# Kernel optimization log

Hardware: AMD Instinct MI355X
Metric: run time of the kernel (lower is better)

Reference implementation:

```python
import jax, jax.numpy as jnp
import numpy as np
from jax import lax


def _gelu(x):
    return jax.nn.gelu(x, approximate=False)  # torch nn.GELU default = exact erf


def _ln_cf(x, g, b, eps=1e-6):
    # channels_first LayerNorm over dim 1 (biased variance, as in the source)
    m = x.mean(1, keepdims=True)
    v = ((x - m) ** 2).mean(1, keepdims=True)
    return g[None, :, None, None] * ((x - m) / jnp.sqrt(v + eps)) + b[None, :, None, None]


def _conv1x1(x, w):
    return jnp.einsum('bihw,oi->bohw', x, w[:, :, 0, 0])


def _conv3x3(x, w, d):
    # 3x3 conv, padding=dilation=d, no bias
    return lax.conv_general_dilated(x, w, (1, 1), [(d, d), (d, d)], rhs_dilation=(d, d),
                                    dimension_numbers=('NCHW', 'OIHW', 'NCHW'))


def _forward(x, conv1_w, conv1_b, conv2_w, conv2_b,
             cw_w1, cw_b1, cw_ln_g, cw_ln_b, cw_w2, cw_b2,
             aspp0_w, aspp0_g, aspp0_b, aspp1_w, aspp1_g, aspp1_b,
             aspp2_w, aspp2_g, aspp2_b, aspp3_w, aspp3_g, aspp3_b,
             asppp_w, asppp_g, asppp_b, proj_w, proj_g, proj_b):
    B, C, H, W = x.shape
    # x1 = conv1(x)
    x1 = _conv1x1(x, conv1_w) + conv1_b[None, :, None, None]
    # ChannelWeighting
    avg = x.mean((2, 3))                                    # [B,C]
    mx = x.max((2, 3))
    o = jnp.abs(avg - mx) * avg
    h = o @ cw_w1.T + cw_b1                                 # [B,Cout]
    mu = h.mean(-1, keepdims=True)
    vv = ((h - mu) ** 2).mean(-1, keepdims=True)
    h = cw_ln_g * ((h - mu) / jnp.sqrt(vv + 1e-5)) + cw_ln_b  # nn.LayerNorm eps=1e-5
    s = jax.nn.sigmoid(h @ cw_w2.T + cw_b2)                 # [B,C]
    xc = x * s[:, :, None, None] + x
    # ASPP (dropout in project is identity at eval)
    b0 = _gelu(_ln_cf(_conv1x1(xc, aspp0_w), aspp0_g, aspp0_b))
    b1 = _gelu(_ln_cf(_conv3x3(xc, aspp1_w, 3), aspp1_g, aspp1_b))
    b2 = _gelu(_ln_cf(_conv3x3(xc, aspp2_w, 6), aspp2_g, aspp2_b))
    b3 = _gelu(_ln_cf(_conv3x3(xc, aspp3_w, 9), aspp3_g, aspp3_b))
    gp = xc.mean((2, 3), keepdims=True)                     # AdaptiveAvgPool2d(1)
    bp = _gelu(_ln_cf(_conv1x1(gp, asppp_w), asppp_g, asppp_b))
    bp = jnp.broadcast_to(bp, (B, C, H, W))                 # bilinear 1x1->HxW == broadcast
    cat = jnp.concatenate([b0, b1, b2, b3, bp], axis=1)     # [B,5C,H,W]
    proj = _gelu(_ln_cf(_conv1x1(cat, proj_w), proj_g, proj_b))
    xa = _conv1x1(proj, conv1_w) + conv1_b[None, :, None, None]
    # AttentionModule, batched (redundant discarded Q@attn from source omitted)
    Co = xa.shape[1]
    HW = H * W
    P = x1.reshape(B, Co, HW)
    Q = xa.reshape(B, Co, HW)
    S = jnp.einsum('bcq,bcp->bqp', Q, P) / jnp.sqrt(jnp.asarray(HW, jnp.float32))
    A = jax.nn.softmax(S, axis=-1)                          # softmax over dim=1 of S[q,p] -> p
    L = jnp.einsum('bck,bkj->bcj', P, A).reshape(B, Co, H, W)
    O = L + xa
    return _conv1x1(O, conv2_w) + conv2_b[None, :, None, None]


def setup_inputs() -> dict:
    key = jax.random.key(0)
    ks = jax.random.split(key, 16)
    Cin, Cout, B, H, W = 256, 128, 4, 64, 64

    def nrm(k, shape, fan):
        return jax.random.normal(k, shape, jnp.float32) / np.float32(np.sqrt(fan))

    return {
        'x': jax.random.normal(ks[0], (B, Cin, H, W), jnp.float32),
        'conv1_w': nrm(ks[1], (Cout, Cin, 1, 1), Cin),
        'conv1_b': jnp.zeros((Cout,), jnp.float32),
        'conv2_w': nrm(ks[2], (Cin, Cout, 1, 1), Cout),
        'conv2_b': jnp.zeros((Cin,), jnp.float32),
        'cw_w1': nrm(ks[3], (Cout, Cin), Cin),
        'cw_b1': jnp.zeros((Cout,), jnp.float32),
        'cw_ln_g': jnp.ones((Cout,), jnp.float32),
        'cw_ln_b': jnp.zeros((Cout,), jnp.float32),
        'cw_w2': nrm(ks[4], (Cin, Cout), Cout),
        'cw_b2': jnp.zeros((Cin,), jnp.float32),
        'aspp0_w': nrm(ks[5], (Cin, Cin, 1, 1), Cin),
        'aspp0_g': jnp.ones((Cin,), jnp.float32),
        'aspp0_b': jnp.zeros((Cin,), jnp.float32),
        'aspp1_w': nrm(ks[6], (Cin, Cin, 3, 3), Cin * 9),
        'aspp1_g': jnp.ones((Cin,), jnp.float32),
        'aspp1_b': jnp.zeros((Cin,), jnp.float32),
        'aspp2_w': nrm(ks[7], (Cin, Cin, 3, 3), Cin * 9),
        'aspp2_g': jnp.ones((Cin,), jnp.float32),
        'aspp2_b': jnp.zeros((Cin,), jnp.float32),
        'aspp3_w': nrm(ks[8], (Cin, Cin, 3, 3), Cin * 9),
        'aspp3_g': jnp.ones((Cin,), jnp.float32),
        'aspp3_b': jnp.zeros((Cin,), jnp.float32),
        'asppp_w': nrm(ks[9], (Cin, Cin, 1, 1), Cin),
        'asppp_g': jnp.ones((Cin,), jnp.float32),
        'asppp_b': jnp.zeros((Cin,), jnp.float32),
        'proj_w': nrm(ks[10], (Cin, 5 * Cin, 1, 1), 5 * Cin),
        'proj_g': jnp.ones((Cin,), jnp.float32),
        'proj_b': jnp.zeros((Cin,), jnp.float32),
    }


def reference(x, conv1_w, conv1_b, conv2_w, conv2_b,
              cw_w1, cw_b1, cw_ln_g, cw_ln_b, cw_w2, cw_b2,
              aspp0_w, aspp0_g, aspp0_b, aspp1_w, aspp1_g, aspp1_b,
              aspp2_w, aspp2_g, aspp2_b, aspp3_w, aspp3_g, aspp3_b,
              asppp_w, asppp_g, asppp_b, proj_w, proj_g, proj_b):
    return _forward(x, conv1_w, conv1_b, conv2_w, conv2_b,
                    cw_w1, cw_b1, cw_ln_g, cw_ln_b, cw_w2, cw_b2,
                    aspp0_w, aspp0_g, aspp0_b, aspp1_w, aspp1_g, aspp1_b,
                    aspp2_w, aspp2_g, aspp2_b, aspp3_w, aspp3_g, aspp3_b,
                    asppp_w, asppp_g, asppp_b, proj_w, proj_g, proj_b)
```

## Files before the change

kernel.cpp:

```cpp
#include <hip/hip_runtime.h>
#include <hip/hip_bf16.h>
#include <math.h>

#define NB 4
#define CI 256
#define CO 128
#define HW 4096

typedef __attribute__((ext_vector_type(8))) short s8v;
typedef __attribute__((ext_vector_type(4))) short s4v;
typedef __attribute__((ext_vector_type(4))) float f4v;

__device__ __forceinline__ unsigned short f2bf(float f){
    __hip_bfloat16 h = __float2bfloat16(f);
    return *reinterpret_cast<unsigned short*>(&h);
}

__device__ __forceinline__ void lds_dma16(const void* g, void* l){
    __builtin_amdgcn_global_load_lds((const __attribute__((address_space(1))) unsigned int*)g,
                                     (__attribute__((address_space(3))) unsigned int*)l,
                                     16, 0, 0);
}

__device__ __forceinline__ float gelu_f(float x){
    float z  = x * 0.70710678118654752f;
    float az = fabsf(z);
    float tt = 1.f / (1.f + 0.3275911f * az);
    float poly = tt*(0.254829592f + tt*(-0.284496736f + tt*(1.421413741f +
                 tt*(-1.453152027f + tt*1.061405429f))));
    float erfv = 1.f - poly * __expf(-az*az);
    erfv = (z < 0.f) ? -erfv : erfv;
    return 0.5f * x * (1.f + erfv);
}

__global__ void k_pre(const float* __restrict__ x, float* __restrict__ avg, float* __restrict__ mx,
                      const float* __restrict__ c1, const float* __restrict__ a0,
                      const float* __restrict__ pj, const float* __restrict__ c2,
                      const float* __restrict__ d3, const float* __restrict__ d6,
                      const float* __restrict__ d9,
                      unsigned short* __restrict__ w_c1, unsigned short* __restrict__ w_a0,
                      unsigned short* __restrict__ w_pj, unsigned short* __restrict__ w_c2,
                      unsigned short* __restrict__ w_d3, unsigned short* __restrict__ w_d6,
                      unsigned short* __restrict__ w_d9){
    int blk = blockIdx.x;
    int t = threadIdx.x;
    if (blk < 1024){
        const float* p = x + (long long)blk * HW;
        float s = 0.f, m = -1e30f;
        for (int i = t; i < HW; i += 256){ float v = p[i]; s += v; m = fmaxf(m, v); }
        __shared__ float ss[256], sm[256];
        ss[t] = s; sm[t] = m; __syncthreads();
        for (int o = 128; o > 0; o >>= 1){
            if (t < o){ ss[t] += ss[t+o]; sm[t] = fmaxf(sm[t], sm[t+o]); }
            __syncthreads();
        }
        if (t == 0){ avg[blk] = ss[0] / (float)HW; mx[blk] = sm[0]; }
        return;
    }
    int i = (blk - 1024)*256 + t;
    if (i < 458752){
        if (i < 32768)        w_c1[i]        = f2bf(c1[i]);
        else if (i < 98304)   w_a0[i-32768]  = f2bf(a0[i-32768]);
        else if (i < 425984)  w_pj[i-98304]  = f2bf(pj[i-98304]);
        else                  w_c2[i-425984] = f2bf(c2[i-425984]);
    } else {
        int j = i - 458752;
        int which = j / 589824;
        int l = j - which*589824;
        int tap = l >> 16, rem = l & 65535, o = rem >> 8, ci = rem & 255;
        const float* src = (which==0) ? d3 : ((which==1) ? d6 : d9);
        unsigned short* dst = (which==0) ? w_d3 : ((which==1) ? w_d6 : w_d9);
        dst[l] = f2bf(src[o*2304 + ci*9 + tap]);
    }
}

__global__ void k_cw(const float* __restrict__ avg, const float* __restrict__ mx,
                     const float* __restrict__ w1, const float* __restrict__ b1,
                     const float* __restrict__ lng, const float* __restrict__ lnb,
                     const float* __restrict__ w2, const float* __restrict__ b2,
                     float* __restrict__ sv, float* __restrict__ gp,
                     float* __restrict__ zb){
    int b = blockIdx.x, t = threadIdx.x;
    if (b == 0) zb[t] = 0.f;
    __shared__ float o_s[256];
    __shared__ float h_s[128];
    __shared__ float stat[2];
    float a = avg[b*256 + t];
    o_s[t] = fabsf(a - mx[b*256 + t]) * a;
    __syncthreads();
    if (t < 128){
        float h = b1[t];
        for (int i = 0; i < 256; i++) h += o_s[i] * w1[t*256 + i];
        h_s[t] = h;
    }
    __syncthreads();
    if (t == 0){
        float s = 0.f, s2 = 0.f;
        for (int j = 0; j < 128; j++){ s += h_s[j]; s2 += h_s[j]*h_s[j]; }
        float mean = s / 128.f;
        float var  = s2 / 128.f - mean*mean;
        stat[0] = mean; stat[1] = rsqrtf(var + 1e-5f);
    }
    __syncthreads();
    if (t < 128) h_s[t] = lng[t] * ((h_s[t] - stat[0]) * stat[1]) + lnb[t];
    __syncthreads();
    float z = b2[t];
    for (int j = 0; j < 128; j++) z += h_s[j] * w2[t*128 + j];
    float sig = 1.f / (1.f + __expf(-z));
    sv[b*256 + t] = sig;
    gp[b*256 + t] = a * (1.f + sig);
}

__global__ void k_xT(const float* __restrict__ x, const float* __restrict__ sv,
                     unsigned short* __restrict__ xT, unsigned short* __restrict__ xcT){
    int b = blockIdx.z, c0 = blockIdx.y*64, h0 = blockIdx.x*64;
    __shared__ unsigned short T1[64][66], T2[64][66];
    int t = threadIdx.x;
    int hl = t & 63, cs = t >> 6;
    #pragma unroll
    for (int r = 0; r < 16; r++){
        int c = cs*16 + r;
        float v = x[((long long)b*256 + c0 + c)*HW + h0 + hl];
        float sc = 1.f + sv[b*256 + c0 + c];
        T1[c][hl] = f2bf(v);
        T2[c][hl] = f2bf(v*sc);
    }
    __syncthreads();
    int cl = t & 63, hs = t >> 6;
    #pragma unroll
    for (int r = 0; r < 16; r++){
        int h = hs*16 + r;
        long long o = ((long long)b*HW + h0 + h)*256 + c0 + cl;
        xT[o]  = T1[cl][h];
        xcT[o] = T2[cl][h];
    }
}

__device__ __forceinline__ void ln_epi32(f4v acc[2][2],
        int b, int n0, int w, int lane, int m, int q, int t,
        const float* Gs, const float* Bts,
        float (*Psum)[32], float (*Psq)[32], float* Mn, float* Iv,
        unsigned short* __restrict__ outT, int outPitch, int colOff){
    float ls[2], ls2[2];
    #pragma unroll
    for (int ct = 0; ct < 2; ct++){
        float s = 0.f, s2 = 0.f;
        #pragma unroll
        for (int ms = 0; ms < 2; ms++)
            #pragma unroll
            for (int r = 0; r < 4; r++){ float v = acc[ms][ct][r]; s += v; s2 += v*v; }
        ls[ct] = s; ls2[ct] = s2;
    }
    #pragma unroll
    for (int ct = 0; ct < 2; ct++){
        ls[ct]  += __shfl_xor(ls[ct], 16);  ls[ct]  += __shfl_xor(ls[ct], 32);
        ls2[ct] += __shfl_xor(ls2[ct], 16); ls2[ct] += __shfl_xor(ls2[ct], 32);
    }
    if (lane < 16){
        #pragma unroll
        for (int ct = 0; ct < 2; ct++){ Psum[w][ct*16+lane] = ls[ct]; Psq[w][ct*16+lane] = ls2[ct]; }
    }
    __syncthreads();
    if (t < 32){
        float s = 0.f, s2 = 0.f;
        #pragma unroll
        for (int ww = 0; ww < 8; ww++){ s += Psum[ww][t]; s2 += Psq[ww][t]; }
        float mean = s * (1.f/256.f);
        Mn[t] = mean;
        Iv[t] = rsqrtf(s2*(1.f/256.f) - mean*mean + 1e-6f);
    }
    __syncthreads();
    #pragma unroll
    for (int ct = 0; ct < 2; ct++){
        int p = ct*16 + m;
        float mean = Mn[p], inv = Iv[p];
        long long rowb = ((long long)b*HW + n0 + p)*outPitch + colOff;
        #pragma unroll
        for (int ms = 0; ms < 2; ms++){
            s4v o4;
            #pragma unroll
            for (int r = 0; r < 4; r++){
                int c = w*32 + ms*16 + q*4 + r;
                float h = Gs[c]*((acc[ms][ct][r] - mean)*inv) + Bts[c];
                o4[r] = (short)f2bf(gelu_f(h));
            }
            *(s4v*)(outT + rowb + w*32 + ms*16 + q*4) = o4;
        }
    }
}

__global__ __launch_bounds__(512, 4)
void k_aspp(const unsigned short* __restrict__ w_a0, const unsigned short* __restrict__ w_d3,
            const unsigned short* __restrict__ w_d6, const unsigned short* __restrict__ w_d9,
            const unsigned short* __restrict__ BT,
            const float* __restrict__ a0_g, const float* __restrict__ a0_b,
            const float* __restrict__ a1_g, const float* __restrict__ a1_b,
            const float* __restrict__ a2_g, const float* __restrict__ a2_b,
            const float* __restrict__ a3_g, const float* __restrict__ a3_b,
            const float* __restrict__ gp, const float* __restrict__ ap_w,
            const float* __restrict__ ap_g, const float* __restrict__ ap_b,
            const float* __restrict__ zbuf,
            unsigned short* __restrict__ catT){
    int br = blockIdx.y, b = blockIdx.z;
    int t = threadIdx.x;
    __shared__ __align__(16) unsigned short As[256*64];
    __shared__ __align__(16) unsigned short Bs[128*64];
    __shared__ float Gs[256], Bts[256];
    if (br == 4){
        int p0 = blockIdx.x*128;
        float* z_s = (float*)As;
        unsigned short* bp_s = As + 2048;
        float* stat = (float*)(As + 4096);
        if (t < 256){
            float z = 0.f;
            for (int c = 0; c < 256; c++) z += gp[b*256 + c] * ap_w[t*256 + c];
            z_s[t] = z;
        }
        __syncthreads();
        if (t == 0){
            float s = 0.f, s2 = 0.f;
            for (int c = 0; c < 256; c++){ s += z_s[c]; s2 += z_s[c]*z_s[c]; }
            float mean = s / 256.f, var = s2 / 256.f - mean*mean;
            stat[0] = mean; stat[1] = rsqrtf(var + 1e-6f);
        }
        __syncthreads();
        if (t < 256){
            float h = ap_g[t] * ((z_s[t] - stat[0]) * stat[1]) + ap_b[t];
            bp_s[t] = f2bf(gelu_f(h));
        }
        __syncthreads();
        for (int it = 0; it < 8; it++){
            int i = it*512 + t;
            int pl = i >> 5, cj = (i & 31) * 8;
            s8v v8;
            #pragma unroll
            for (int k2 = 0; k2 < 8; k2++) v8[k2] = (short)bp_s[cj + k2];
            *(s8v*)(catT + ((long long)b*HW + p0 + pl)*1280 + 1024 + cj) = v8;
        }
        return;
    }
    int n0 = blockIdx.x * 128;
    const unsigned short* BTb = BT + (long long)b*HW*256;
    const unsigned short* A  = (br==0) ? w_a0 : (br==1) ? w_d3 : (br==2) ? w_d6 : w_d9;
    const float* g   = (br==0) ? a0_g : (br==1) ? a1_g : (br==2) ? a2_g : a3_g;
    const float* bta = (br==0) ? a0_b : (br==1) ? a1_b : (br==2) ? a2_b : a3_b;
    int d    = (br==0) ? 0 : (br==1) ? 3 : (br==2) ? 6 : 9;
    int NS   = (br==0) ? 4 : 36;
    if (t < 256){ Gs[t] = g[t]; Bts[t] = bta[t]; }

    int w = t>>6, lane = t&63, m = lane&15, q = lane>>4;
    int wr = w>>1, wc = w&1;
    int rsw = m&7;
    int rl8 = lane>>3;
    int gch = (lane&7) ^ rl8;
    int aoff = rl8*256 + gch*8;
    int y0 = n0 >> 6;

    f4v acc[4][4];
    #pragma unroll
    for (int ms = 0; ms < 4; ms++)
        #pragma unroll
        for (int ct = 0; ct < 4; ct++){ f4v z = {0.f,0.f,0.f,0.f}; acc[ms][ct] = z; }

    for (int s = 0; s < NS; ++s){
        int tap = s>>2, kc = s&3;
        int dy = tap/3 - 1, dx = tap%3 - 1;
        const unsigned short* abase = A + tap*65536 + kc*64 + aoff;
        #pragma unroll
        for (int i = 0; i < 4; i++){
            int row0 = w*32 + i*8;
            lds_dma16(abase + row0*256, &As[row0*64]);
        }
        int xadd = rl8 + dx*d;
        #pragma unroll
        for (int i = 0; i < 2; i++){
            int bn0 = w*16 + i*8;
            int yy = y0 + (bn0>>6) + dy*d;
            int xs = (bn0 & 63) + xadd;
            const unsigned short* gsrc = ((unsigned)yy < 64u && (unsigned)xs < 64u)
                ? (BTb + (long long)(yy*64 + xs)*256 + kc*64 + gch*8)
                : (const unsigned short*)zbuf;
            lds_dma16(gsrc, &Bs[bn0*64]);
        }
        __syncthreads();
        #pragma unroll
        for (int ks = 0; ks < 2; ks++){
            s8v bfr[4];
            #pragma unroll
            for (int ct = 0; ct < 4; ct++)
                bfr[ct] = *(const s8v*)&Bs[(wc*64 + ct*16 + m)*64 + ((q + 4*ks) ^ rsw)*8];
            #pragma unroll
            for (int ms = 0; ms < 4; ms++){
                s8v afr = *(const s8v*)&As[(wr*64 + ms*16 + m)*64 + ((q + 4*ks) ^ rsw)*8];
                #pragma unroll
                for (int ct = 0; ct < 4; ct++)
                    acc[ms][ct] = __builtin_amdgcn_mfma_f32_16x16x32_bf16(afr, bfr[ct], acc[ms][ct], 0,0,0);
            }
        }
        __syncthreads();
    }
    float* Psum = (float*)Bs;
    float* Psq  = Psum + 512;
    float* Mn   = Psq  + 512;
    float* Iv   = Mn   + 128;
    #pragma unroll
    for (int ct = 0; ct < 4; ct++){
        float s = 0.f, s2 = 0.f;
        #pragma unroll
        for (int ms = 0; ms < 4; ms++)
            #pragma unroll
            for (int r = 0; r < 4; r++){ float v = acc[ms][ct][r]; s += v; s2 += v*v; }
        s  += __shfl_xor(s, 16);  s  += __shfl_xor(s, 32);
        s2 += __shfl_xor(s2, 16); s2 += __shfl_xor(s2, 32);
        if (lane < 16){
            Psum[wr*128 + wc*64 + ct*16 + lane] = s;
            Psq [wr*128 + wc*64 + ct*16 + lane] = s2;
        }
    }
    __syncthreads();
    if (t < 128){
        float s  = Psum[t] + Psum[128+t] + Psum[256+t] + Psum[384+t];
        float s2 = Psq [t] + Psq [128+t] + Psq [256+t] + Psq [384+t];
        float mean = s * (1.f/256.f);
        Mn[t] = mean;
        Iv[t] = rsqrtf(s2*(1.f/256.f) - mean*mean + 1e-6f);
    }
    __syncthreads();
    #pragma unroll
    for (int ct = 0; ct < 4; ct++){
        int p = wc*64 + ct*16 + m;
        float mean = Mn[p], inv = Iv[p];
        long long rowb = ((long long)b*HW + n0 + p)*1280 + br*256;
        #pragma unroll
        for (int ms = 0; ms < 4; ms++){
            s4v o4;
            #pragma unroll
            for (int r = 0; r < 4; r++){
                int c = wr*64 + ms*16 + q*4 + r;
                float h = Gs[c]*((acc[ms][ct][r] - mean)*inv) + Bts[c];
                o4[r] = (short)f2bf(gelu_f(h));
            }
            *(s4v*)(catT + rowb + wr*64 + ms*16 + q*4) = o4;
        }
    }
}

__global__ __launch_bounds__(512)
void k_branch1(const unsigned short* __restrict__ A, int K,
               const unsigned short* __restrict__ BT,
               const float* __restrict__ g, const float* __restrict__ beta,
               unsigned short* __restrict__ outT, int outPitch, int colOff){
    int b = blockIdx.y, n0 = blockIdx.x*32;
    const unsigned short* BTb = BT + (long long)b*HW*K;
    __shared__ __align__(16) unsigned short As[256*64];
    __shared__ __align__(16) unsigned short Bs[32*64];
    __shared__ float Psum[8][32], Psq[8][32], Mn[32], Iv[32];
    __shared__ float Gs[256], Bts[256];
    int t = threadIdx.x, w = t>>6, lane = t&63, m = lane&15, q = lane>>4;
    int rl8 = lane>>3, gch = (lane&7) ^ rl8, rsw = m&7;
    if (t < 256){ Gs[t] = g[t]; Bts[t] = beta[t]; }
    f4v acc[2][2];
    #pragma unroll
    for (int ms = 0; ms < 2; ms++)
        #pragma unroll
        for (int ct = 0; ct < 2; ct++){ f4v z = {0.f,0.f,0.f,0.f}; acc[ms][ct] = z; }
    for (int k0 = 0; k0 < K; k0 += 64){
        #pragma unroll
        for (int i = 0; i < 4; i++){
            int ar = w*32 + i*8;
            lds_dma16(A + (long long)(ar + rl8)*K + k0 + gch*8, &As[ar*64]);
        }
        if (w < 4){
            int brr = w*8;
            lds_dma16(BTb + (long long)(n0 + brr + rl8)*K + k0 + gch*8, &Bs[brr*64]);
        }
        __syncthreads();
        #pragma unroll
        for (int ks = 0; ks < 2; ks++){
            s8v bfr[2];
            #pragma unroll
            for (int ct = 0; ct < 2; ct++)
                bfr[ct] = *(const s8v*)&Bs[(ct*16 + m)*64 + ((q + 4*ks) ^ rsw)*8];
            #pragma unroll
            for (int ms = 0; ms < 2; ms++){
                s8v afr = *(const s8v*)&As[(w*32 + ms*16 + m)*64 + ((q + 4*ks) ^ rsw)*8];
                #pragma unroll
                for (int ct = 0; ct < 2; ct++)
                    acc[ms][ct] = __builtin_amdgcn_mfma_f32_16x16x32_bf16(afr, bfr[ct], acc[ms][ct], 0,0,0);
            }
        }
        __syncthreads();
    }
    ln_epi32(acc, b, n0, w, lane, m, q, t, Gs, Bts, Psum, Psq, Mn, Iv, outT, outPitch, colOff);
}

__global__ __launch_bounds__(256)
void k_conv1m(const unsigned short* __restrict__ A,
              const unsigned short* __restrict__ BT,
              const float* __restrict__ bias,
              unsigned short* __restrict__ outT,
              unsigned short* __restrict__ outC,
              float* __restrict__ outF){
    int b = blockIdx.y, n0 = blockIdx.x*32;
    const unsigned short* BTb = BT + (long long)b*HW*256;
    __shared__ __align__(16) unsigned short As[128*64];
    __shared__ __align__(16) unsigned short Bs[32*64];
    int t = threadIdx.x, w = t>>6, lane = t&63, m = lane&15, q = lane>>4;
    int rl8 = lane>>3, gch = (lane&7) ^ rl8, rsw = m&7;
    f4v acc[2][2];
    #pragma unroll
    for (int ms = 0; ms < 2; ms++)
        #pragma unroll
        for (int ct = 0; ct < 2; ct++){ f4v z = {0.f,0.f,0.f,0.f}; acc[ms][ct] = z; }
    for (int k0 = 0; k0 < 256; k0 += 64){
        #pragma unroll
        for (int i = 0; i < 4; i++){
            int ar = w*32 + i*8;
            lds_dma16(A + (long long)(ar + rl8)*256 + k0 + gch*8, &As[ar*64]);
        }
        lds_dma16(BTb + (long long)(n0 + w*8 + rl8)*256 + k0 + gch*8, &Bs[w*8*64]);
        __syncthreads();
        #pragma unroll
        for (int ks = 0; ks < 2; ks++){
            s8v bfr[2];
            #pragma unroll
            for (int ct = 0; ct < 2; ct++)
                bfr[ct] = *(const s8v*)&Bs[(ct*16 + m)*64 + ((q + 4*ks) ^ rsw)*8];
            #pragma unroll
            for (int ms = 0; ms < 2; ms++){
                s8v afr = *(const s8v*)&As[(w*32 + ms*16 + m)*64 + ((q + 4*ks) ^ rsw)*8];
                #pragma unroll
                for (int ct = 0; ct < 2; ct++)
                    acc[ms][ct] = __builtin_amdgcn_mfma_f32_16x16x32_bf16(afr, bfr[ct], acc[ms][ct], 0,0,0);
            }
        }
        __syncthreads();
    }
    #pragma unroll
    for (int ct = 0; ct < 2; ct++){
        int p = n0 + ct*16 + m;
        #pragma unroll
        for (int ms = 0; ms < 2; ms++){
            s4v o4;
            float vals[4];
            #pragma unroll
            for (int r = 0; r < 4; r++){
                int c = w*32 + ms*16 + q*4 + r;
                vals[r] = acc[ms][ct][r] + bias[c];
                o4[r] = (short)f2bf(vals[r]);
            }
            *(s4v*)(outT + ((long long)b*HW + p)*128 + w*32 + ms*16 + q*4) = o4;
            if (outC){
                #pragma unroll
                for (int r = 0; r < 4; r++){
                    int c = w*32 + ms*16 + q*4 + r;
                    outC[((long long)b*128 + c)*HW + p] = (unsigned short)o4[r];
                }
            }
            if (outF){
                #pragma unroll
                for (int r = 0; r < 4; r++){
                    int c = w*32 + ms*16 + q*4 + r;
                    outF[((long long)b*128 + c)*HW + p] = vals[r];
                }
            }
        }
    }
}

__global__ __launch_bounds__(256)
void k_attn_stats3(const unsigned short* __restrict__ QT,
                   const unsigned short* __restrict__ PT,
                   float* __restrict__ lpart){
    int b = blockIdx.z, jc = blockIdx.y, k0 = blockIdx.x * 128;
    const unsigned short* QTb = QT + (long long)b * HW * CO;
    const unsigned short* PTb = PT + (long long)b * HW * CO;
    __shared__ unsigned short Ps[2][64][132];
    int t = threadIdx.x;
    int w = t >> 6, lane = t & 63, m = lane & 15, q = lane >> 4;
    s8v a[2][4];
    #pragma unroll
    for (int kh = 0; kh < 2; kh++)
        #pragma unroll
        for (int ks = 0; ks < 4; ks++)
            a[kh][ks] = *(const s8v*)(QTb + (long long)(k0 + kh*64 + w*16 + m) * CO + q*8 + ks*32);
    float rl[2][4];
    #pragma unroll
    for (int kh = 0; kh < 2; kh++)
        #pragma unroll
        for (int r = 0; r < 4; r++) rl[kh][r] = 0.f;
    const float scale = 0.015625f;
    int jbase = jc * 1024;
    int sr = t >> 2, sch = t & 3;
    uint4 pf[4];
    {   const uint4* src = (const uint4*)(PTb + (long long)(jbase + sr) * CO + sch * 32);
        #pragma unroll
        for (int i = 0; i < 4; i++) pf[i] = src[i];
    }
    for (int jt = 0; jt < 16; jt++){
        int cur = jt & 1;
        {   uint4* dst = (uint4*)&Ps[cur][sr][sch * 32];
            #pragma unroll
            for (int i = 0; i < 4; i++) dst[i] = pf[i];
        }
        __syncthreads();
        if (jt < 15){
            const uint4* src = (const uint4*)(PTb + (long long)(jbase + (jt+1)*64 + sr) * CO + sch * 32);
            #pragma unroll
            for (int i = 0; i < 4; i++) pf[i] = src[i];
        }
        #pragma unroll
        for (int kh = 0; kh < 2; kh++){
            float sv[4][4];
            #pragma unroll
            for (int ct = 0; ct < 4; ct++){
                f4v acc = {0.f,0.f,0.f,0.f};
                #pragma unroll
                for (int ks = 0; ks < 4; ks++){
                    s8v bv = *(const s8v*)&Ps[cur][ct*16 + m][q*8 + ks*32];
                    acc = __builtin_amdgcn_mfma_f32_16x16x32_bf16(a[kh][ks], bv, acc, 0, 0, 0);
                }
                #pragma unroll
                for (int r = 0; r < 4; r++) sv[ct][r] = acc[r] * scale;
            }
            #pragma unroll
            for (int r = 0; r < 4; r++){
                float se = __expf(sv[0][r]) + __expf(sv[1][r])
                         + __expf(sv[2][r]) + __expf(sv[3][r]);
                #pragma unroll
                for (int msk = 1; msk < 16; msk <<= 1) se += __shfl_xor(se, msk);
                rl[kh][r] += se;
            }
        }
    }
    if (m == 0){
        #pragma unroll
        for (int kh = 0; kh < 2; kh++)
            #pragma unroll
            for (int r = 0; r < 4; r++){
                int k = k0 + kh*64 + w*16 + q*4 + r;
                lpart[(long long)jc * (NB*HW) + (long long)b*HW + k] = rl[kh][r];
            }
    }
}

__global__ __launch_bounds__(256)
void k_attn_apply2(const unsigned short* __restrict__ QT,
                   const unsigned short* __restrict__ PT,
                   const unsigned short* __restrict__ Pb,
                   const float* __restrict__ lpart,
                   float* __restrict__ Lp){
    int b = blockIdx.z, kc = blockIdx.y, j0 = blockIdx.x * 64;
    const unsigned short* QTb = QT + (long long)b * HW * CO;
    const unsigned short* PTb = PT + (long long)b * HW * CO;
    const unsigned short* Pbb = Pb + (long long)b * CO * HW;
    __shared__ __align__(16) unsigned short Qks[64*128];
    __shared__ __align__(16) unsigned short Pcs[128*64];
    __shared__ unsigned short Et[64][72];
    __shared__ float Il[2048];
    int t = threadIdx.x;
    int w = t >> 6, lane = t & 63, m = lane & 15, q = lane >> 4;
    int kbase = kc * 2048;
    int rl4 = lane >> 4;
    int rl8 = lane >> 3;
    int gch8 = (lane & 7) ^ rl8;
    {
        #pragma unroll
        for (int r = 0; r < 8; r++){
            int kl = t*8 + r;
            long long gi = (long long)b*HW + kbase + kl;
            float l = lpart[gi] + lpart[gi+16384] + lpart[gi+32768] + lpart[gi+49152];
            Il[kl] = 1.f / l;
        }
    }
    {
        #pragma unroll
        for (int i = 0; i < 4; i++){
            int rowb = w*16 + i*4;
            int gch = (lane & 15) ^ ((rowb & 15) + rl4);
            lds_dma16(PTb + (long long)(j0 + rowb + rl4)*CO + gch*8, &Qks[rowb*128]);
        }
    }
    __syncthreads();
    s8v bj[4][4];
    #pragma unroll
    for (int ct = 0; ct < 4; ct++)
        #pragma unroll
        for (int ks = 0; ks < 4; ks++)
            bj[ct][ks] = *(const s8v*)&Qks[(ct*16 + m)*128 + ((q + 4*ks) ^ m)*8];
    f4v accL[2][4];
    #pragma unroll
    for (int mt = 0; mt < 2; mt++)
        #pragma unroll
        for (int ct = 0; ct < 4; ct++){ f4v z = {0.f,0.f,0.f,0.f}; accL[mt][ct] = z; }
    const float scale = 0.015625f;
    for (int kt = 0; kt < 32; kt++){
        int k0 = kbase + kt*64;
        __syncthreads();
        {
            #pragma unroll
            for (int i = 0; i < 4; i++){
                int rowb = w*16 + i*4;
                int gch = (lane & 15) ^ ((rowb & 15) + rl4);
                lds_dma16(QTb + (long long)(k0 + rowb + rl4)*CO + gch*8, &Qks[rowb*128]);
            }
        }
        {
            #pragma unroll
            for (int i = 0; i < 4; i++){
                int rowb = w*32 + i*8;
                lds_dma16(Pbb + (long long)(rowb + rl8)*HW + k0 + gch8*8, &Pcs[rowb*64]);
            }
        }
        __syncthreads();
        s8v aS[4];
        #pragma unroll
        for (int ks = 0; ks < 4; ks++)
            aS[ks] = *(const s8v*)&Qks[(w*16 + m)*128 + ((q + 4*ks) ^ m)*8];
        float il[4];
        #pragma unroll
        for (int r = 0; r < 4; r++) il[r] = Il[kt*64 + w*16 + q*4 + r];
        #pragma unroll
        for (int ct = 0; ct < 4; ct++){
            f4v s = {0.f,0.f,0.f,0.f};
            #pragma unroll
            for (int ks = 0; ks < 4; ks++)
                s = __builtin_amdgcn_mfma_f32_16x16x32_bf16(aS[ks], bj[ct][ks], s, 0, 0, 0);
            s4v e4;
            #pragma unroll
            for (int r = 0; r < 4; r++)
                e4[r] = (short)f2bf(__expf(s[r]*scale) * il[r]);
            *(s4v*)&Et[ct*16 + m][w*16 + q*4] = e4;
        }
        __syncthreads();
        s8v aP[2][2];
        #pragma unroll
        for (int mt = 0; mt < 2; mt++)
            #pragma unroll
            for (int ks2 = 0; ks2 < 2; ks2++)
                aP[mt][ks2] = *(const s8v*)&Pcs[(w*32 + mt*16 + m)*64 + ((q + 4*ks2) ^ (m&7))*8];
        #pragma unroll
        for (int ct = 0; ct < 4; ct++){
            s8v bE0 = *(const s8v*)&Et[ct*16 + m][q*8];
            s8v bE1 = *(const s8v*)&Et[ct*16 + m][q*8 + 32];
            #pragma unroll
            for (int mt = 0; mt < 2; mt++){
                accL[mt][ct] = __builtin_amdgcn_mfma_f32_16x16x32_bf16(aP[mt][0], bE0, accL[mt][ct], 0, 0, 0);
                accL[mt][ct] = __builtin_amdgcn_mfma_f32_16x16x32_bf16(aP[mt][1], bE1, accL[mt][ct], 0, 0, 0);
            }
        }
    }
    float* Lpb = Lp + ((long long)(kc*NB + b) * CO) * HW;
    #pragma unroll
    for (int mt = 0; mt < 2; mt++)
        #pragma unroll
        for (int ct = 0; ct < 4; ct++)
            #pragma unroll
            for (int r = 0; r < 4; r++){
                int c = w*32 + mt*16 + q*4 + r;
                Lpb[(long long)c*HW + j0 + ct*16 + m] = accL[mt][ct][r];
            }
}

__global__ __launch_bounds__(256)
void k_outfused(const unsigned short* __restrict__ A,
                const float* __restrict__ Lp, const float* __restrict__ xa,
                const float* __restrict__ bias, float* __restrict__ out){
    int b = blockIdx.y, j0 = blockIdx.x*32;
    __shared__ unsigned short Bs[32][136];
    __shared__ __align__(16) char pool[256*68*2];
    int t = threadIdx.x;
    {
        float* Bsf = (float*)pool;
        int c = t>>1, jh = t&1;
        long long base = ((long long)b*CO + c)*HW + j0 + jh*16;
        const long long csz = (long long)NB*CO*HW;
        float v[16];
        #pragma unroll
        for (int r = 0; r < 16; r++) v[r] = xa[base + r];
        #pragma unroll
        for (int pidx = 0; pidx < 2; pidx++){
            const float* src = Lp + pidx*csz + base;
            #pragma unroll
            for (int r = 0; r < 16; r++) v[r] += src[r];
        }
        #pragma unroll
        for (int r = 0; r < 16; r++) Bsf[c*33 + jh*16 + r] = v[r];
    }
    __syncthreads();
    {
        const float* Bsf = (const float*)pool;
        int j = t>>3, cs = t&7;
        #pragma unroll
        for (int r = 0; r < 16; r++){
            int c = cs*16 + r;
            Bs[j][c] = f2bf(Bsf[c*33 + j]);
        }
    }
    __syncthreads();
    unsigned short* As = (unsigned short*)pool;
    int w = t>>6, lane = t&63, m = lane&15, q = lane>>4;
    int rl8 = lane>>3, gch = (lane&7) ^ rl8, rsw = m&7;
    f4v acc[4][2];
    #pragma unroll
    for (int ms = 0; ms < 4; ms++)
        #pragma unroll
        for (int ct = 0; ct < 2; ct++){ f4v z = {0.f,0.f,0.f,0.f}; acc[ms][ct] = z; }
    for (int k0 = 0; k0 < 128; k0 += 64){
        __syncthreads();
        #pragma unroll
        for (int i = 0; i < 8; i++){
            int ar = w*64 + i*8;
            lds_dma16(A + (long long)(ar + rl8)*128 + k0 + gch*8, &As[ar*64]);
        }
        __syncthreads();
        #pragma unroll
        for (int ks = 0; ks < 2; ks++){
            s8v bfr[2];
            #pragma unroll
            for (int ct = 0; ct < 2; ct++) bfr[ct] = *(const s8v*)&Bs[ct*16+m][k0 + ks*32 + q*8];
            #pragma unroll
            for (int ms = 0; ms < 4; ms++){
                s8v afr = *(const s8v*)&As[(w*64 + ms*16 + m)*64 + ((q + 4*ks) ^ rsw)*8];
                #pragma unroll
                for (int ct = 0; ct < 2; ct++)
                    acc[ms][ct] = __builtin_amdgcn_mfma_f32_16x16x32_bf16(afr, bfr[ct], acc[ms][ct], 0,0,0);
            }
        }
    }
    #pragma unroll
    for (int ct = 0; ct < 2; ct++){
        int p = j0 + ct*16 + m;
        #pragma unroll
        for (int ms = 0; ms < 4; ms++)
            #pragma unroll
            for (int r = 0; r < 4; r++){
                int c = w*64 + ms*16 + q*4 + r;
                out[((long long)b*256 + c)*HW + p] = acc[ms][ct][r] + bias[c];
            }
    }
}

extern "C" void kernel_launch(void* const* d_in, const int* in_sizes, int n_in,
                              void* d_out, int out_size, void* d_ws, size_t ws_size,
                              hipStream_t stream) {
    const float* x       = (const float*)d_in[0];
    const float* conv1_w = (const float*)d_in[1];
    const float* conv1_b = (const float*)d_in[2];
    const float* conv2_w = (const float*)d_in[3];
    const float* conv2_b = (const float*)d_in[4];
    const float* cw_w1   = (const float*)d_in[5];
    const float* cw_b1   = (const float*)d_in[6];
    const float* cw_g    = (const float*)d_in[7];
    const float* cw_bt   = (const float*)d_in[8];
    const float* cw_w2   = (const float*)d_in[9];
    const float* cw_b2   = (const float*)d_in[10];
    const float* a0_w    = (const float*)d_in[11];
    const float* a0_g    = (const float*)d_in[12];
    const float* a0_b    = (const float*)d_in[13];
    const float* a1_w    = (const float*)d_in[14];
    const float* a1_g    = (const float*)d_in[15];
    const float* a1_b    = (const float*)d_in[16];
    const float* a2_w    = (const float*)d_in[17];
    const float* a2_g    = (const float*)d_in[18];
    const float* a2_b    = (const float*)d_in[19];
    const float* a3_w    = (const float*)d_in[20];
    const float* a3_g    = (const float*)d_in[21];
    const float* a3_b    = (const float*)d_in[22];
    const float* ap_w    = (const float*)d_in[23];
    const float* ap_g    = (const float*)d_in[24];
    const float* ap_b    = (const float*)d_in[25];
    const float* pj_w    = (const float*)d_in[26];
    const float* pj_g    = (const float*)d_in[27];
    const float* pj_b    = (const float*)d_in[28];
    float* out = (float*)d_out;

    float* ws    = (float*)d_ws;
    float* avg   = ws;
    float* mx    = ws + 1024;
    float* sv    = ws + 2048;
    float* gp    = ws + 3072;
    float* zbuf  = ws + 4096;
    float* xa    = ws + 37888;
    float* lpart = xa + 2097152;
    unsigned short* sb = (unsigned short*)(ws + 4232192);
    unsigned short* xT    = sb;
    unsigned short* xcT   = sb + 4194304;
    unsigned short* catT  = sb + 8388608;
    unsigned short* projT = sb + 29360128;
    unsigned short* P_bf  = sb + 33554432;
    unsigned short* PT_bf = sb + 35651584;
    unsigned short* QT_bf = sb + 37748736;
    unsigned short* w_c1  = sb + 41943040;
    unsigned short* w_a0  = sb + 41975808;
    unsigned short* w_pj  = sb + 42041344;
    unsigned short* w_c2  = sb + 42369024;
    unsigned short* w_d3  = sb + 42401792;
    unsigned short* w_d6  = sb + 42991616;
    unsigned short* w_d9  = sb + 43581440;
    float* Lp = (float*)catT;

    k_pre<<<dim3(9728), 256, 0, stream>>>(x, avg, mx,
                                          conv1_w, a0_w, pj_w, conv2_w, a1_w, a2_w, a3_w,
                                          w_c1, w_a0, w_pj, w_c2, w_d3, w_d6, w_d9);
    k_cw<<<dim3(NB), 256, 0, stream>>>(avg, mx, cw_w1, cw_b1, cw_g, cw_bt, cw_w2, cw_b2, sv, gp, zbuf);

    k_xT<<<dim3(64, 4, NB), 256, 0, stream>>>(x, sv, xT, xcT);

    k_conv1m<<<dim3(128, NB), 256, 0, stream>>>(w_c1, xT, conv1_b, PT_bf, P_bf, nullptr);

    k_aspp<<<dim3(32, 5, NB), 512, 0, stream>>>(w_a0, w_d3, w_d6, w_d9, xcT,
                                                a0_g, a0_b, a1_g, a1_b, a2_g, a2_b, a3_g, a3_b,
                                                gp, ap_w, ap_g, ap_b, zbuf, catT);

    k_branch1<<<dim3(128, NB), 512, 0, stream>>>(w_pj, 1280, catT, pj_g, pj_b, projT, 256, 0);

    k_conv1m<<<dim3(128, NB), 256, 0, stream>>>(w_c1, projT, conv1_b, QT_bf, nullptr, xa);

    k_attn_stats3<<<dim3(32, 4, NB), 256, 0, stream>>>(QT_bf, PT_bf, lpart);
    k_attn_apply2<<<dim3(64, 2, NB), 256, 0, stream>>>(QT_bf, PT_bf, P_bf, lpart, Lp);

    k_outfused<<<dim3(128, NB), 256, 0, stream>>>(w_c2, Lp, xa, conv2_b, out);

    (void)in_sizes; (void)n_in; (void)out_size; (void)ws_size;
}
```

Baseline: 391.1 us.

## Double-buffer branch1 GEMM loads and software-pipeline attention-like loop prefetches

k_branch1 now double-buffers its A/B LDS tiles and issues the next stage's async global-to-LDS loads before computing the current one, using explicit vmcnt waits and raw barriers in place of full syncthreads. The second kernel interleaves prefetch of the next Q and P tiles with the current stage's MFMA work, so each single-buffered tile is reloaded as soon as its consumer phase finishes. The aim is to hide global load latency behind MFMA compute. In exchange, branch1's LDS use roughly doubles, which may cut occupancy, and the hand-counted vmcnt values are fragile and easy to get wrong.

```diff
diff --git a/kernel.cpp b/kernel.cpp
--- a/kernel.cpp
+++ b/kernel.cpp
@@ -352,8 +352,8 @@
                unsigned short* __restrict__ outT, int outPitch, int colOff){
     int b = blockIdx.y, n0 = blockIdx.x*32;
     const unsigned short* BTb = BT + (long long)b*HW*K;
-    __shared__ __align__(16) unsigned short As[256*64];
-    __shared__ __align__(16) unsigned short Bs[32*64];
+    __shared__ __align__(16) unsigned short As[2][256*64];
+    __shared__ __align__(16) unsigned short Bs[2][32*64];
     __shared__ float Psum[8][32], Psq[8][32], Mn[32], Iv[32];
     __shared__ float Gs[256], Bts[256];
     int t = threadIdx.x, w = t>>6, lane = t&63, m = lane&15, q = lane>>4;
@@ -364,33 +364,49 @@
     for (int ms = 0; ms < 2; ms++)
         #pragma unroll
         for (int ct = 0; ct < 2; ct++){ f4v z = {0.f,0.f,0.f,0.f}; acc[ms][ct] = z; }
-    for (int k0 = 0; k0 < K; k0 += 64){
+    const int NSt = K >> 6;
+    auto issue = [&](int s, int buf){
+        int k0 = s*64;
         #pragma unroll
         for (int i = 0; i < 4; i++){
             int ar = w*32 + i*8;
-            lds_dma16(A + (long long)(ar + rl8)*K + k0 + gch*8, &As[ar*64]);
-        }
-        if (w < 4){
-            int brr = w*8;
-            lds_dma16(BTb + (long long)(n0 + brr + rl8)*K + k0 + gch*8, &Bs[brr*64]);
-        }
-        __syncthreads();
+            lds_dma16(A + (long long)(ar + rl8)*K + k0 + gch*8, &As[buf][ar*64]);
+        }
+        if (w < 4)
+            lds_dma16(BTb + (long long)(n0 + w*8 + rl8)*K + k0 + gch*8, &Bs[buf][w*8*64]);
+    };
+    issue(0, 0);
+    for (int s = 0; s < NSt; ++s){
+        int cur = s & 1;
+        if (s+1 < NSt){
+            issue(s+1, cur^1);
+            if (w < 4) asm volatile("s_waitcnt vmcnt(5)" ::: "memory");
+            else       asm volatile("s_waitcnt vmcnt(4)" ::: "memory");
+        } else {
+            asm volatile("s_waitcnt vmcnt(0)" ::: "memory");
+        }
+        __builtin_amdgcn_s_barrier();
+        __builtin_amdgcn_sched_barrier(0);
+        const unsigned short* Ac = &As[cur][0];
+        const unsigned short* Bc = &Bs[cur][0];
         #pragma unroll
         for (int ks = 0; ks < 2; ks++){
             s8v bfr[2];
             #pragma unroll
             for (int ct = 0; ct < 2; ct++)
-                bfr[ct] = *(const s8v*)&Bs[(ct*16 + m)*64 + ((q + 4*ks) ^ rsw)*8];
+                bfr[ct] = *(const s8v*)&Bc[(ct*16 + m)*64 + ((q + 4*ks) ^ rsw)*8];
             #pragma unroll
             for (int ms = 0; ms < 2; ms++){
-                s8v afr = *(const s8v*)&As[(w*32 + ms*16 + m)*64 + ((q + 4*ks) ^ rsw)*8];
+                s8v afr = *(const s8v*)&Ac[(w*32 + ms*16 + m)*64 + ((q + 4*ks) ^ rsw)*8];
                 #pragma unroll
                 for (int ct = 0; ct < 2; ct++)
                     acc[ms][ct] = __builtin_amdgcn_mfma_f32_16x16x32_bf16(afr, bfr[ct], acc[ms][ct], 0,0,0);
             }
         }
-        __syncthreads();
-    }
+        __builtin_amdgcn_s_barrier();
+        __builtin_amdgcn_sched_barrier(0);
+    }
+    __syncthreads();
     ln_epi32(acc, b, n0, w, lane, m, q, t, Gs, Bts, Psum, Psq, Mn, Iv, outT, outPitch, colOff);
 }
 
@@ -580,14 +596,32 @@
             int gch = (lane & 15) ^ ((rowb & 15) + rl4);
             lds_dma16(PTb + (long long)(j0 + rowb + rl4)*CO + gch*8, &Qks[rowb*128]);
         }
-    }
-    __syncthreads();
+        #pragma unroll
+        for (int i = 0; i < 4; i++){
+            int rowb = w*32 + i*8;
+            lds_dma16(Pbb + (long long)(rowb + rl8)*HW + kbase + gch8*8, &Pcs[rowb*64]);
+        }
+    }
+    asm volatile("s_waitcnt vmcnt(4) lgkmcnt(0)" ::: "memory");
+    __builtin_amdgcn_s_barrier();
+    __builtin_amdgcn_sched_barrier(0);
     s8v bj[4][4];
     #pragma unroll
     for (int ct = 0; ct < 4; ct++)
         #pragma unroll
         for (int ks = 0; ks < 4; ks++)
             bj[ct][ks] = *(const s8v*)&Qks[(ct*16 + m)*128 + ((q + 4*ks) ^ m)*8];
+    asm volatile("s_waitcnt lgkmcnt(0)" ::: "memory");
+    __builtin_amdgcn_s_barrier();
+    __builtin_amdgcn_sched_barrier(0);
+    {
+        #pragma unroll
+        for (int i = 0; i < 4; i++){
+            int rowb = w*16 + i*4;
+            int gch = (lane & 15) ^ ((rowb & 15) + rl4);
+            lds_dma16(QTb + (long long)(kbase + rowb + rl4)*CO + gch*8, &Qks[rowb*128]);
+        }
+    }
     f4v accL[2][4];
     #pragma unroll
     for (int mt = 0; mt < 2; mt++)
@@ -596,43 +630,41 @@
     const float scale = 0.015625f;
     for (int kt = 0; kt < 32; kt++){
         int k0 = kbase + kt*64;
-        __syncthreads();
-        {
+        if (kt == 0) asm volatile("s_waitcnt vmcnt(0)" ::: "memory");
+        else         asm volatile("s_waitcnt vmcnt(4)" ::: "memory");
+        __builtin_amdgcn_sched_barrier(0);
+        s8v aS[4];
+        #pragma unroll
+        for (int ks = 0; ks < 4; ks++)
+            aS[ks] = *(const s8v*)&Qks[(w*16 + m)*128 + ((q + 4*ks) ^ m)*8];
+        float il[4];
+        #pragma unroll
+        for (int r = 0; r < 4; r++) il[r] = Il[kt*64 + w*16 + q*4 + r];
+        #pragma unroll
+        for (int ct = 0; ct < 4; ct++){
+            f4v s = {0.f,0.f,0.f,0.f};
+            #pragma unroll
+            for (int ks = 0; ks < 4; ks++)
+                s = __builtin_amdgcn_mfma_f32_16x16x32_bf16(aS[ks], bj[ct][ks], s, 0, 0, 0);
+            s4v e4;
+            #pragma unroll
+            for (int r = 0; r < 4; r++)
+                e4[r] = (short)f2bf(__expf(s[r]*scale) * il[r]);
+            *(s4v*)&Et[ct*16 + m][w*16 + q*4] = e4;
+        }
+        if (kt+1 < 32){
             #pragma unroll
             for (int i = 0; i < 4; i++){
                 int rowb = w*16 + i*4;
                 int gch = (lane & 15) ^ ((rowb & 15) + rl4);
-                lds_dma16(QTb + (long long)(k0 + rowb + rl4)*CO + gch*8, &Qks[rowb*128]);
-            }
-        }
-        {
-            #pragma unroll
-            for (int i = 0; i < 4; i++){
-                int rowb = w*32 + i*8;
-                lds_dma16(Pbb + (long long)(rowb + rl8)*HW + k0 + gch8*8, &Pcs[rowb*64]);
-            }
-        }
-        __syncthreads();
-        s8v aS[4];
-        #pragma unroll
-        for (int ks = 0; ks < 4; ks++)
-            aS[ks] = *(const s8v*)&Qks[(w*16 + m)*128 + ((q + 4*ks) ^ m)*8];
-        float il[4];
-        #pragma unroll
-        for (int r = 0; r < 4; r++) il[r] = Il[kt*64 + w*16 + q*4 + r];
-        #pragma unroll
-        for (int ct = 0; ct < 4; ct++){
-            f4v s = {0.f,0.f,0.f,0.f};
-            #pragma unroll
-            for (int ks = 0; ks < 4; ks++)
-                s = __builtin_amdgcn_mfma_f32_16x16x32_bf16(aS[ks], bj[ct][ks], s, 0, 0, 0);
-            s4v e4;
-            #pragma unroll
-            for (int r = 0; r < 4; r++)
-                e4[r] = (short)f2bf(__expf(s[r]*scale) * il[r]);
-            *(s4v*)&Et[ct*16 + m][w*16 + q*4] = e4;
-        }
-        __syncthreads();
+                lds_dma16(QTb + (long long)(k0 + 64 + rowb + rl4)*CO + gch*8, &Qks[rowb*128]);
+            }
+        }
+        asm volatile("s_waitcnt lgkmcnt(0)" ::: "memory");
+        __builtin_amdgcn_s_barrier();
+        __builtin_amdgcn_sched_barrier(0);
+        asm volatile("s_waitcnt vmcnt(4)" ::: "memory");
+        __builtin_amdgcn_sched_barrier(0);
         s8v aP[2][2];
         #pragma unroll
         for (int mt = 0; mt < 2; mt++)
@@ -649,6 +681,15 @@
                 accL[mt][ct] = __builtin_amdgcn_mfma_f32_16x16x32_bf16(aP[mt][1], bE1, accL[mt][ct], 0, 0, 0);
             }
         }
+        if (kt+1 < 32){
+            #pragma unroll
+            for (int i = 0; i < 4; i++){
+                int rowb = w*32 + i*8;
+                lds_dma16(Pbb + (long long)(rowb + rl8)*HW + k0 + 64 + gch8*8, &Pcs[rowb*64]);
+            }
+        }
+        __builtin_amdgcn_s_barrier();
+        __builtin_amdgcn_sched_barrier(0);
     }
     float* Lpb = Lp + ((long long)(kc*NB + b) * CO) * HW;
     #pragma unroll
```

Result: faster. 375.1 us (-4.1%).
